# Kernel optimization log

Hardware: AMD Instinct MI355X
Metric: run time of the kernel (lower is better)

## Reference

```python
import jax, jax.numpy as jnp
import numpy as np

EMBED_DIM = 1024
NUM_HEADS = 16
HEAD_DIM = EMBED_DIM // NUM_HEADS
N_PATCHES = 220
ROPE_BASE = 10000.0
EPS = 1e-6


def rms_norm(x, g):
    # x: [..., d]
    rms = jnp.sqrt(jnp.mean(x * x, axis=-1, keepdims=True) + EPS)
    return g * (x / rms)


def apply_rope(x):
    # torchtune-style interleaved RoPE. x: [b, s, h, d]
    b, s, h, d = x.shape
    theta = 1.0 / (ROPE_BASE ** (jnp.arange(0, d, 2, dtype=jnp.float32) / d))  # [d/2]
    ang = jnp.arange(s, dtype=jnp.float32)[:, None] * theta[None, :]           # [s, d/2]
    cos = jnp.cos(ang)[None, :, None, :]
    sin = jnp.sin(ang)[None, :, None, :]
    xs = x.reshape(b, s, h, d // 2, 2)
    x0, x1 = xs[..., 0], xs[..., 1]
    out = jnp.stack([x0 * cos - x1 * sin, x1 * cos + x0 * sin], axis=-1)
    return out.reshape(b, s, h, d).astype(x.dtype)


def attention_block(x, w_qkv, w_proj, b_proj, q_gain, k_gain):
    # x: [N, S, C]; one SDPA branch (shared by spatial & temporal paths)
    N, S, C = x.shape
    H, D = NUM_HEADS, HEAD_DIM
    qkv = jnp.einsum('nsc,ec->nse', x, w_qkv).reshape(N, S, 3, H, D)
    q, k, v = qkv[:, :, 0], qkv[:, :, 1], qkv[:, :, 2]  # [N, S, H, D]
    q = apply_rope(rms_norm(q, q_gain))
    k = apply_rope(rms_norm(k, k_gain))
    scale = 1.0 / jnp.sqrt(jnp.float32(D))
    scores = jnp.einsum('nqhd,nkhd->nhqk', q, k) * scale
    attn = jax.nn.softmax(scores, axis=-1)
    out = jnp.einsum('nhqk,nkhd->nqhd', attn, v).reshape(N, S, C)
    return jnp.einsum('nsc,ec->nse', out, w_proj) + b_proj


def setup_inputs() -> dict:
    key = jax.random.key(0)
    ks = jax.random.split(key, 8)
    E = EMBED_DIM
    sd = 1.0 / np.sqrt(E)
    x = jax.random.normal(ks[0], (4, 5280, E), dtype=jnp.float32)
    w_sqkv = jax.random.uniform(ks[1], (3 * E, E), jnp.float32, -sd, sd)
    w_sproj = jax.random.uniform(ks[2], (E, E), jnp.float32, -sd, sd)
    b_sproj = jax.random.uniform(ks[3], (E,), jnp.float32, -sd, sd)
    w_tqkv = jax.random.uniform(ks[4], (3 * E, E), jnp.float32, -sd, sd)
    w_tproj = jax.random.uniform(ks[5], (E, E), jnp.float32, -sd, sd)
    b_tproj = jax.random.uniform(ks[6], (E,), jnp.float32, -sd, sd)
    g = jnp.ones((HEAD_DIM,), jnp.float32)
    return {
        'x': x,
        'w_sqkv': w_sqkv, 'w_sproj': w_sproj, 'b_sproj': b_sproj,
        'w_tqkv': w_tqkv, 'w_tproj': w_tproj, 'b_tproj': b_tproj,
        'sq_gain': g, 'sk_gain': g, 'tq_gain': g, 'tk_gain': g,
    }


def reference(x, w_sqkv, w_sproj, b_sproj, w_tqkv, w_tproj, b_tproj,
              sq_gain, sk_gain, tq_gain, tk_gain):
    B, T, C = x.shape
    P = N_PATCHES
    F = T // P
    # spatial attention per frame: (b f) p c
    xs = x.reshape(B, F, P, C).reshape(B * F, P, C)
    out_s = attention_block(xs, w_sqkv, w_sproj, b_sproj, sq_gain, sk_gain)
    # temporal attention per patch: (b p) f c
    xt = out_s.reshape(B, F, P, C).transpose(0, 2, 1, 3).reshape(B * P, F, C)
    out_t = attention_block(xt, w_tqkv, w_tproj, b_tproj, tq_gain, tk_gain)
    # (b p) f c -> b (f p) c
    out = out_t.reshape(B, P, F, C).transpose(0, 2, 1, 3).reshape(B, F * P, C)
    return out
```

## Files before the change

### kernel.cpp

```cpp
#include <hip/hip_runtime.h>

typedef _Float16 f16;
typedef _Float16 f16x8 __attribute__((ext_vector_type(8)));
typedef f16x8 f16x8a __attribute__((may_alias));
typedef float f32x4 __attribute__((ext_vector_type(4)));

#define NTOK 21120
#define MPAD 21248
#define SCALE_Q 0.18033688f

__device__ __forceinline__ void gll16(const void* g, void* l) {
  __builtin_amdgcn_global_load_lds(
      (const __attribute__((address_space(1))) unsigned int*)g,
      (__attribute__((address_space(3))) unsigned int*)l, 16, 0, 0);
}

__device__ __forceinline__ unsigned int pack2(float a, float b) {
  union { f16 h[2]; unsigned int u; } c;
  c.h[0] = (f16)a; c.h[1] = (f16)b;
  return c.u;
}
__device__ __forceinline__ unsigned short f2h(float a) {
  union { f16 h; unsigned short u; } c; c.h = (f16)a; return c.u;
}

template <int C>
__device__ __forceinline__ float dppf(float x) {
  union { float f; int i; } u, r;
  u.f = x;
  r.i = __builtin_amdgcn_update_dpp(0, u.i, C, 0xf, 0xf, true);
  return r.f;
}

__global__ __launch_bounds__(256) void cast_kernel(
    const float* __restrict__ in, unsigned short* __restrict__ out, int n4) {
  int i = blockIdx.x * 256 + threadIdx.x;
  if (i >= n4) return;
  float4 v = ((const float4*)in)[i];
  uint2 o;
  o.x = pack2(v.x, v.y);
  o.y = pack2(v.z, v.w);
  ((uint2*)out)[i] = o;
}

__global__ __launch_bounds__(256) void transpose_cast_kernel(
    const float* __restrict__ in, unsigned short* __restrict__ out) {
  __shared__ float tile[32][33];
  int bx = blockIdx.x & 31, by = blockIdx.x >> 5;
  int tx = threadIdx.x & 31, ty = threadIdx.x >> 5;
#pragma unroll
  for (int i = 0; i < 32; i += 8)
    tile[ty + i][tx] = in[(size_t)(by * 32 + ty + i) * 1024 + bx * 32 + tx];
  __syncthreads();
#pragma unroll
  for (int i = 0; i < 32; i += 8)
    out[(size_t)(bx * 32 + ty + i) * 1024 + by * 32 + tx] = f2h(tile[tx][ty + i]);
}

__global__ __launch_bounds__(256) void bias_combine_kernel(
    const float* __restrict__ w, const float* __restrict__ b, float* __restrict__ bc) {
  int e = blockIdx.x * 256 + threadIdx.x;
  if (e >= 3072) return;
  const float4* wr = (const float4*)(w + (size_t)e * 1024);
  const float4* b4 = (const float4*)b;
  float s = 0.f;
  for (int c = 0; c < 256; ++c) {
    float4 wv = wr[c], bv = b4[c];
    s += wv.x * bv.x + wv.y * bv.y + wv.z * bv.z + wv.w * bv.w;
  }
  bc[e] = s;
}

__global__ __launch_bounds__(256) void rope_table_kernel(float2* tabS, float2* tabT) {
  int t = blockIdx.x * 256 + threadIdx.x;
  const float lb = logf(10000.0f) * (1.0f / 32.0f);
  if (t < 220 * 32) {
    int s = t >> 5, i = t & 31;
    float theta = expf(-(float)i * lb);
    float ang = (float)s * theta;
    tabS[t] = make_float2(cosf(ang), sinf(ang));
  } else if (t < 220 * 32 + 24 * 32) {
    int u = t - 220 * 32;
    int s = u >> 5, i = u & 31;
    float theta = expf(-(float)i * lb);
    float ang = (float)s * theta;
    tabT[u] = make_float2(cosf(ang), sinf(ang));
  }
}

__global__ __launch_bounds__(256) void gemm_bt(
    const unsigned short* __restrict__ A, const unsigned short* __restrict__ B,
    const float* __restrict__ bias, void* __restrict__ C,
    int M, int N, int K, int outmode,
    const float2* __restrict__ tab, const float* __restrict__ gq,
    const float* __restrict__ gk, int mode) {
  __shared__ __align__(16) unsigned short sh[16384];
  unsigned short* As = sh;
  unsigned short* Bs = sh + 8192;
  const int tid = threadIdx.x;
  const int w = tid >> 6, lane = tid & 63;
  const int l15 = lane & 15, quad = lane >> 4;
  const int wr = w >> 1, wc = w & 1;

  const int ntn = N >> 7;
  const int stride = ntn << 3;
  const int g = blockIdx.x / stride, r = blockIdx.x % stride;
  const int tn = r % ntn, tm = g * 8 + r / ntn;

  f32x4 acc[4][4];
#pragma unroll
  for (int a = 0; a < 4; ++a)
#pragma unroll
    for (int b = 0; b < 4; ++b) acc[a][b] = (f32x4){0.f, 0.f, 0.f, 0.f};

  const int srow = tid >> 3;
  const int schk = tid & 7;
  const size_t arow0 = (size_t)tm * 128;
  const size_t brow0 = (size_t)tn * 128;
  const int nk = K >> 6;

  for (int kt = 0; kt < nk; ++kt) {
    __syncthreads();
    const int kb = kt << 6;
#pragma unroll
    for (int rd = 0; rd < 4; ++rd) {
      int row = rd * 32 + srow;
      int sc = (schk ^ (row & 7)) * 8;
      gll16(A + (arow0 + row) * K + kb + sc, (char*)As + rd * 4096 + tid * 16);
      gll16(B + (brow0 + row) * K + kb + sc, (char*)Bs + rd * 4096 + tid * 16);
    }
    __syncthreads();
#pragma unroll
    for (int kk = 0; kk < 2; ++kk) {
      f16x8 af[4], bf[4];
#pragma unroll
      for (int mt = 0; mt < 4; ++mt) {
        int ra = wr * 64 + mt * 16 + l15;
        af[mt] = *(const f16x8a*)((const char*)As + ra * 128 + (((kk * 4 + quad) ^ (ra & 7)) * 16));
        int rb = wc * 64 + mt * 16 + l15;
        bf[mt] = *(const f16x8a*)((const char*)Bs + rb * 128 + (((kk * 4 + quad) ^ (rb & 7)) * 16));
      }
#pragma unroll
      for (int mt = 0; mt < 4; ++mt)
#pragma unroll
        for (int nt = 0; nt < 4; ++nt)
          acc[mt][nt] = __builtin_amdgcn_mfma_f32_16x16x32_f16(af[mt], bf[nt], acc[mt][nt], 0, 0, 0);
    }
  }

  unsigned short* Cs = (unsigned short*)C;
#pragma unroll
  for (int p = 0; p < 2; ++p) {
    __syncthreads();
#pragma unroll
    for (int mi = 0; mi < 2; ++mi) {
      int mt = p * 2 + mi;
      int rl = wr * 32 + mi * 16 + quad * 4;
#pragma unroll
      for (int nt = 0; nt < 4; ++nt) {
        int cl = wc * 64 + nt * 16 + l15;
#pragma unroll
        for (int rg = 0; rg < 4; ++rg)
          sh[(rl + rg) * 136 + cl] = f2h(acc[mt][nt][rg]);
      }
    }
    __syncthreads();
#pragma unroll
    for (int c = 0; c < 4; ++c) {
      int rl = c * 16 + (tid >> 4), cx = tid & 15;
      int grow = tm * 128 + ((rl >> 5) << 6) + p * 32 + (rl & 31);
      uint4 v = *(const uint4*)&sh[rl * 136 + cx * 8];
      *(uint4*)&Cs[(size_t)grow * N + tn * 128 + cx * 8] = v;
    }
  }
}

#define FENCE() asm volatile("" ::: "memory")
#define BAR() do { FENCE(); __builtin_amdgcn_s_barrier(); FENCE(); } while (0)
#define WAITV(N) asm volatile("s_waitcnt vmcnt(" #N ")" ::: "memory")
#define WAITL(N) do { asm volatile("s_waitcnt lgkmcnt(" #N ")" ::: "memory"); \
                      __builtin_amdgcn_sched_barrier(0); } while (0)
#define ASLOT(T) (((T) % 3) * 32768)
#define BSLOT(T) (98304 + ((T) & 1) * 32768)
#define LDAf(T, mt, kk) (*(const f16x8a*)(smem + ASLOT(T) + wrOff + (mt) * 2048 + (aoff ^ ((kk) << 6))))
#define LDBf(T, nt, kk) (*(const f16x8a*)(smem + BSLOT(T) + bcOff + (nt) * 2048 + (aoff ^ ((kk) << 6))))
#define STAGE_A2(T, h) do { \
    gll16(aSp + (size_t)((h) * 128) * K + (T) * 64, smem + ASLOT(T) + (h) * 16384 + tid * 16); \
    gll16(aSp + (size_t)((h) * 128 + 64) * K + (T) * 64, smem + ASLOT(T) + (h) * 16384 + 8192 + tid * 16); \
  } while (0)
#define STAGE_B2(T, h) do { \
    gll16(bSp + (size_t)((h) * 128) * K + (T) * 64, smem + BSLOT(T) + (h) * 16384 + tid * 16); \
    gll16(bSp + (size_t)((h) * 128 + 64) * K + (T) * 64, smem + BSLOT(T) + (h) * 16384 + 8192 + tid * 16); \
  } while (0)
#define MM16(QB, A0_, A1_, A2_, A3_, B0_, B1_, B2_, B3_) do { \
    acc[QB + 0][0] = __builtin_amdgcn_mfma_f32_16x16x32_f16(A0_, B0_, acc[QB + 0][0], 0, 0, 0); \
    acc[QB + 0][1] = __builtin_amdgcn_mfma_f32_16x16x32_f16(A0_, B1_, acc[QB + 0][1], 0, 0, 0); \
    acc[QB + 0][2] = __builtin_amdgcn_mfma_f32_16x16x32_f16(A0_, B2_, acc[QB + 0][2], 0, 0, 0); \
    acc[QB + 0][3] = __builtin_amdgcn_mfma_f32_16x16x32_f16(A0_, B3_, acc[QB + 0][3], 0, 0, 0); \
    acc[QB + 1][0] = __builtin_amdgcn_mfma_f32_16x16x32_f16(A1_, B0_, acc[QB + 1][0], 0, 0, 0); \
    acc[QB + 1][1] = __builtin_amdgcn_mfma_f32_16x16x32_f16(A1_, B1_, acc[QB + 1][1], 0, 0, 0); \
    acc[QB + 1][2] = __builtin_amdgcn_mfma_f32_16x16x32_f16(A1_, B2_, acc[QB + 1][2], 0, 0, 0); \
    acc[QB + 1][3] = __builtin_amdgcn_mfma_f32_16x16x32_f16(A1_, B3_, acc[QB + 1][3], 0, 0, 0); \
    acc[QB + 2][0] = __builtin_amdgcn_mfma_f32_16x16x32_f16(A2_, B0_, acc[QB + 2][0], 0, 0, 0); \
    acc[QB + 2][1] = __builtin_amdgcn_mfma_f32_16x16x32_f16(A2_, B1_, acc[QB + 2][1], 0, 0, 0); \
    acc[QB + 2][2] = __builtin_amdgcn_mfma_f32_16x16x32_f16(A2_, B2_, acc[QB + 2][2], 0, 0, 0); \
    acc[QB + 2][3] = __builtin_amdgcn_mfma_f32_16x16x32_f16(A2_, B3_, acc[QB + 2][3], 0, 0, 0); \
    acc[QB + 3][0] = __builtin_amdgcn_mfma_f32_16x16x32_f16(A3_, B0_, acc[QB + 3][0], 0, 0, 0); \
    acc[QB + 3][1] = __builtin_amdgcn_mfma_f32_16x16x32_f16(A3_, B1_, acc[QB + 3][1], 0, 0, 0); \
    acc[QB + 3][2] = __builtin_amdgcn_mfma_f32_16x16x32_f16(A3_, B2_, acc[QB + 3][2], 0, 0, 0); \
    acc[QB + 3][3] = __builtin_amdgcn_mfma_f32_16x16x32_f16(A3_, B3_, acc[QB + 3][3], 0, 0, 0); \
  } while (0)

__global__ __launch_bounds__(512, 2) void gemm256(
    const unsigned short* __restrict__ A, const unsigned short* __restrict__ B,
    const float* __restrict__ bias, void* __restrict__ C,
    int M, int N, int K, int outmode,
    const float2* __restrict__ tab, const float* __restrict__ gq,
    const float* __restrict__ gk, int mode) {
  extern __shared__ char smem[];
  const int tid = threadIdx.x;
  const int w = tid >> 6, lane = tid & 63;
  const int l15 = lane & 15, quad = lane >> 4;
  const int wr = w >> 2, wc = w & 3;

  const int nwg = gridDim.x;
  const int qd = nwg >> 3, rm = nwg & 7;
  const int xcd = blockIdx.x & 7, lin = blockIdx.x >> 3;
  const int wgid = (xcd < rm ? xcd * (qd + 1) : rm * (qd + 1) + (xcd - rm) * qd) + lin;
  const int ntn = N >> 8;
  const int stg = ntn << 3;
  const int g = wgid / stg, r2 = wgid % stg;
  const int tn = r2 % ntn, tm = g * 8 + r2 / ntn;

  const int wrOff = wr * 16384;
  const int bcOff = (wc >> 1) * 16384 + (wc & 1) * 8192;
  const int aoff = l15 * 128 + ((quad ^ (l15 & 7)) << 4);

  const int sc = ((tid & 7) ^ ((tid >> 3) & 7)) * 8;
  const unsigned short* aSp = A + (size_t)(tm * 256 + (tid >> 3)) * K + sc;
  const unsigned short* bSp = B + (size_t)(tn * 256 + (tid >> 3)) * K + sc;

  f32x4 acc[8][4];
#pragma unroll
  for (int i = 0; i < 8; ++i)
#pragma unroll
    for (int j = 0; j < 4; ++j) acc[i][j] = (f32x4){0.f, 0.f, 0.f, 0.f};

  STAGE_A2(0, 0); STAGE_A2(0, 1);
  STAGE_B2(0, 0); STAGE_B2(0, 1);
  STAGE_A2(1, 0); STAGE_A2(1, 1);
  WAITV(4);
  BAR();

#pragma unroll
  for (int t = 0; t < 16; ++t) {
    f16x8 bA0, bA1, bA2, bA3, bB0, bB1, bB2, bB3;
    f16x8 aA0, aA1, aA2, aA3, aB0, aB1, aB2, aB3;
    f16x8 aC0, aC1, aC2, aC3, aD0, aD1, aD2, aD3;
    bA0 = LDBf(t, 0, 0); bA1 = LDBf(t, 1, 0); bA2 = LDBf(t, 2, 0); bA3 = LDBf(t, 3, 0);
    aA0 = LDAf(t, 0, 0); aA1 = LDAf(t, 1, 0); aA2 = LDAf(t, 2, 0); aA3 = LDAf(t, 3, 0);
    aB0 = LDAf(t, 4, 0); aB1 = LDAf(t, 5, 0); aB2 = LDAf(t, 6, 0); aB3 = LDAf(t, 7, 0);
    if (t <= 14) { STAGE_B2(t + 1, 0); STAGE_B2(t + 1, 1); }
    WAITL(4);
    __builtin_amdgcn_s_setprio(1);
    MM16(0, aA0, aA1, aA2, aA3, bA0, bA1, bA2, bA3);
    __builtin_amdgcn_s_setprio(0);
    bB0 = LDBf(t, 0, 1); bB1 = LDBf(t, 1, 1); bB2 = LDBf(t, 2, 1); bB3 = LDBf(t, 3, 1);
    aC0 = LDAf(t, 0, 1); aC1 = LDAf(t, 1, 1); aC2 = LDAf(t, 2, 1); aC3 = LDAf(t, 3, 1);
    WAITL(8);
    __builtin_amdgcn_s_setprio(1);
    MM16(4, aB0, aB1, aB2, aB3, bA0, bA1, bA2, bA3);
    __builtin_amdgcn_s_setprio(0);
    aD0 = LDAf(t, 4, 1); aD1 = LDAf(t, 5, 1); aD2 = LDAf(t, 6, 1); aD3 = LDAf(t, 7, 1);
    if (t <= 13) { STAGE_A2(t + 2, 0); STAGE_A2(t + 2, 1); }
    WAITL(4);
    __builtin_amdgcn_s_setprio(1);
    MM16(0, aC0, aC1, aC2, aC3, bB0, bB1, bB2, bB3);
    __builtin_amdgcn_s_setprio(0);
    WAITL(0);
    __builtin_amdgcn_s_setprio(1);
    MM16(4, aD0, aD1, aD2, aD3, bB0, bB1, bB2, bB3);
    __builtin_amdgcn_s_setprio(0);
    if (t <= 13) { WAITV(4); } else if (t == 14) { WAITV(0); }
    BAR();
  }

  const size_t grow0 = (size_t)tm * 256 + wr * 128;
  const int gcol0 = tn * 256 + wc * 64;

  float bl[4] = {0.f, 0.f, 0.f, 0.f};
  if (bias != nullptr) {
#pragma unroll
    for (int nt = 0; nt < 4; ++nt) bl[nt] = bias[gcol0 + nt * 16 + l15];
  }

  if (outmode == 2) {
    float* wf = (float*)(smem + w * 16384);
    const int frow = lane >> 4, fc = lane & 15;
#pragma unroll
    for (int h = 0; h < 2; ++h) {
#pragma unroll
      for (int mi = 0; mi < 4; ++mi)
#pragma unroll
        for (int nt = 0; nt < 4; ++nt)
#pragma unroll
          for (int rg = 0; rg < 4; ++rg) {
            int row = mi * 16 + quad * 4 + rg;
            int col = nt * 16 + l15;
            int c = col >> 2, lo = col & 3;
            wf[row * 64 + ((c ^ (row & 15)) << 2) + lo] = acc[h * 4 + mi][nt][rg] + bl[nt];
          }
#pragma unroll
      for (int it = 0; it < 16; ++it) {
        int row = it * 4 + frow;
        float4 v = *(const float4*)(wf + row * 64 + ((fc ^ (row & 15)) << 2));
        size_t gr = grow0 + h * 64 + row;
        if (gr < (size_t)M)
          *(float4*)((float*)C + gr * N + gcol0 + fc * 4) = v;
      }
    }
    return;
  }

  unsigned short* wh = (unsigned short*)(smem + w * 16384);
  if (outmode == 3 && tn < 8) {
    const int isQ = tn < 4;
    const float* gg = isQ ? gq : gk;
    float gv[4];
#pragma unroll
    for (int nt = 0; nt < 4; ++nt) gv[nt] = gg[nt * 16 + l15];
#pragma unroll
    for (int mt = 0; mt < 8; ++mt) {
      float v[4][4], rr[4];
#pragma unroll
      for (int rg = 0; rg < 4; ++rg) rr[rg] = 0.f;
#pragma unroll
      for (int nt = 0; nt < 4; ++nt)
#pragma unroll
        for (int rg = 0; rg < 4; ++rg) {
          float x = acc[mt][nt][rg] + bl[nt];
          v[nt][rg] = x;
          rr[rg] += x * x;
        }
#pragma unroll
      for (int rg = 0; rg < 4; ++rg) {
        float s = rr[rg];
        s += dppf<0xB1>(s);
        s += dppf<0x4E>(s);
        s += dppf<0x141>(s);
        s += dppf<0x140>(s);
        float r = rsqrtf(s * (1.0f / 64.0f) + 1e-6f);
        rr[rg] = isQ ? r * SCALE_Q : r;
      }
      int pos[4];
#pragma unroll
      for (int rg = 0; rg < 4; ++rg) {
        int grow = (int)grow0 + mt * 16 + quad * 4 + rg;
        pos[rg] = mode ? ((grow / 220) % 24) : (grow % 220);
      }
#pragma unroll
      for (int nt = 0; nt < 4; ++nt) {
        int col = nt * 16 + l15;
        int ii = nt * 8 + (l15 >> 1);
        int c = col >> 3, lo = col & 7;
#pragma unroll
        for (int rg = 0; rg < 4; ++rg) {
          float2 cs = tab[pos[rg] * 32 + ii];
          float x = v[nt][rg] * rr[rg] * gv[nt];
          float p = dppf<0xB1>(x);
          float o = (l15 & 1) ? (x * cs.x + p * cs.y) : (x * cs.x - p * cs.y);
          int row = mt * 16 + quad * 4 + rg;
          wh[row * 64 + ((c ^ (row & 7)) << 3) + lo] = f2h(o);
        }
      }
    }
  } else {
#pragma unroll
    for (int mt = 0; mt < 8; ++mt)
#pragma unroll
      for (int nt = 0; nt < 4; ++nt) {
        int col = nt * 16 + l15;
        int c = col >> 3, lo = col & 7;
#pragma unroll
        for (int rg = 0; rg < 4; ++rg) {
          int row = mt * 16 + quad * 4 + rg;
          wh[row * 64 + ((c ^ (row & 7)) << 3) + lo] = f2h(acc[mt][nt][rg] + bl[nt]);
        }
      }
  }
  {
    const int frow = lane >> 3, fch = lane & 7;
    unsigned short* C16 = (unsigned short*)C;
#pragma unroll
    for (int it = 0; it < 16; ++it) {
      int row = it * 8 + frow;
      uint4 vv = *(const uint4*)((const char*)wh + row * 128 + ((fch ^ (row & 7)) << 4));
      size_t gr = grow0 + row;
      if (gr < (size_t)M)
        *(uint4*)(C16 + gr * N + gcol0 + fch * 8) = vv;
    }
  }
}

__global__ __launch_bounds__(256) void attn_spatial(
    const unsigned short* __restrict__ qkv, unsigned short* __restrict__ aout) {
  __shared__ __align__(16) unsigned short sh[30720];
  unsigned short* Kls = sh;
  unsigned short* Vt = sh + 8192;
  unsigned short* P = sh + 22528;
  const int tid = threadIdx.x;
  const int w = tid >> 6, lane = tid & 63;
  const int l15 = lane & 15, quad = lane >> 4;
  const int n = blockIdx.x >> 4, h = blockIdx.x & 15;
  const size_t tb = (size_t)n * 220;
  const unsigned short* qbase = qkv + tb * 3072 + h * 64;

  f16x8 aq[4][2];
#pragma unroll
  for (int mt = 0; mt < 4; ++mt) {
    int row = w * 64 + mt * 16 + l15;
    if (row > 219) row = 219;
#pragma unroll
    for (int c = 0; c < 2; ++c)
      aq[mt][c] = *(const f16x8a*)(qbase + (size_t)row * 3072 + c * 32 + quad * 8);
  }
  if (tid < 220) {
    const uint4* src = (const uint4*)(qbase + (size_t)tid * 3072 + 2048);
    uint4 vv[8];
#pragma unroll
    for (int c = 0; c < 8; ++c) vv[c] = src[c];
    const unsigned short* us = (const unsigned short*)vv;
#pragma unroll
    for (int d = 0; d < 64; ++d) Vt[d * 224 + tid] = us[d];
  } else if (tid < 224) {
#pragma unroll
    for (int d = 0; d < 64; ++d) Vt[d * 224 + tid] = 0;
  }

  float lsum[4][4];
  f32x4 o[4][4];
#pragma unroll
  for (int mt = 0; mt < 4; ++mt)
#pragma unroll
    for (int rg = 0; rg < 4; ++rg) lsum[mt][rg] = 0.f;
#pragma unroll
  for (int mt = 0; mt < 4; ++mt)
#pragma unroll
    for (int nt = 0; nt < 4; ++nt) o[mt][nt] = (f32x4){0.f, 0.f, 0.f, 0.f};

  const int xr = (l15 & 3) ^ ((l15 >> 2) & 3);
  unsigned short* Pw = P + w * 2048;

  for (int half = 0; half < 2; ++half) {
    const int k0 = half * 128;
    const int nslot = half ? 736 : 1024;
#pragma unroll
    for (int k = 0; k < 4; ++k) {
      int slot = k * 256 + tid;
      if (slot < nslot) {
        int rl = slot >> 3, c = slot & 7;
        gll16(qbase + (size_t)(k0 + rl) * 3072 + 1024 + ((c ^ (rl & 7)) * 8),
              (char*)Kls + k * 4096 + w * 1024);
      }
    }
    __syncthreads();
    const int nci = half ? 3 : 4;
    for (int ci = 0; ci < nci; ++ci) {
      const int cig = half * 4 + ci;
      f16x8 bk[2][2];
#pragma unroll
      for (int ct = 0; ct < 2; ++ct) {
        int rl = ci * 32 + ct * 16 + l15;
#pragma unroll
        for (int c = 0; c < 2; ++c)
          bk[ct][c] = *(const f16x8a*)((const char*)Kls + rl * 128 + (((quad + 4 * c) ^ (rl & 7)) * 16));
      }
      f32x4 sc[4][2];
#pragma unroll
      for (int mt = 0; mt < 4; ++mt)
#pragma unroll
        for (int ct = 0; ct < 2; ++ct) {
          f32x4 z = (f32x4){0.f, 0.f, 0.f, 0.f};
          z = __builtin_amdgcn_mfma_f32_16x16x32_f16(aq[mt][0], bk[ct][0], z, 0, 0, 0);
          sc[mt][ct] = __builtin_amdgcn_mfma_f32_16x16x32_f16(aq[mt][1], bk[ct][1], z, 0, 0, 0);
        }
      const int okk = (cig * 32 + 16 + l15) < 220;
#pragma unroll
      for (int mt = 0; mt < 4; ++mt)
#pragma unroll
        for (int rg = 0; rg < 4; ++rg) {
          float p0 = exp2f(sc[mt][0][rg]);
          float p1 = okk ? exp2f(sc[mt][1][rg]) : 0.0f;
          lsum[mt][rg] += p0 + p1;
          int xw = quad ^ rg;
          unsigned short* pb = Pw + (mt * 16 + quad * 4 + rg) * 32;
          pb[(((l15 >> 3) ^ xw) * 8) + (l15 & 7)] = f2h(p0);
          pb[(((2 + (l15 >> 3)) ^ xw) * 8) + (l15 & 7)] = f2h(p1);
        }
      __asm__ volatile("s_waitcnt lgkmcnt(0)" ::: "memory");
      f16x8 ap[4], bv[4];
#pragma unroll
      for (int mt = 0; mt < 4; ++mt)
        ap[mt] = *(const f16x8a*)((const char*)Pw + (mt * 16 + l15) * 64 + (quad ^ xr) * 16);
#pragma unroll
      for (int nt = 0; nt < 4; ++nt)
        bv[nt] = *(const f16x8a*)((const char*)Vt + (nt * 16 + l15) * 448 + cig * 64 + quad * 16);
#pragma unroll
      for (int mt = 0; mt < 4; ++mt)
#pragma unroll
        for (int nt = 0; nt < 4; ++nt)
          o[mt][nt] = __builtin_amdgcn_mfma_f32_16x16x32_f16(ap[mt], bv[nt], o[mt][nt], 0, 0, 0);
    }
    __syncthreads();
  }

#pragma unroll
  for (int mt = 0; mt < 4; ++mt)
#pragma unroll
    for (int rg = 0; rg < 4; ++rg) {
      float l = lsum[mt][rg];
      l += __shfl_xor(l, 1);
      l += __shfl_xor(l, 2);
      l += __shfl_xor(l, 4);
      l += __shfl_xor(l, 8);
      int s = w * 64 + mt * 16 + quad * 4 + rg;
      if (s < 220) {
        float inv = 1.0f / l;
        unsigned short* dst = aout + (tb + s) * 1024 + h * 64;
#pragma unroll
        for (int nt = 0; nt < 4; ++nt) dst[nt * 16 + l15] = f2h(o[mt][nt][rg] * inv);
      }
    }
}

__global__ __launch_bounds__(256) void attn_temporal(
    const unsigned short* __restrict__ qkv, unsigned short* __restrict__ aout) {
  __shared__ __align__(16) unsigned short sh[14336];
  const int tid = threadIdx.x;
  const int w = tid >> 6, lane = tid & 63;
  const int l15 = lane & 15, quad = lane >> 4;
  const int b = blockIdx.x / 880;
  const int rem = blockIdx.x % 880;
  const int p = rem >> 2, hq = rem & 3;
  const int h = hq * 4 + w;
  unsigned short* Vtw = sh + w * 2560;
  unsigned short* Pw = sh + 10240 + w * 1024;
  const unsigned short* base = qkv + ((size_t)(b * 24) * 220 + p) * 3072 + h * 64;
  const size_t fs = (size_t)220 * 3072;

  {
    int r = lane >> 1, hf = lane & 1;
    if (r < 24) {
      const uint4* src = (const uint4*)(base + r * fs + 2048 + hf * 32);
      uint4 vv[4];
#pragma unroll
      for (int c = 0; c < 4; ++c) vv[c] = src[c];
      const unsigned short* us = (const unsigned short*)vv;
#pragma unroll
      for (int j = 0; j < 32; ++j) Vtw[(hf * 32 + j) * 40 + r] = us[j];
    } else {
#pragma unroll
      for (int j = 0; j < 32; ++j) Vtw[(hf * 32 + j) * 40 + r] = 0;
    }
  }
  f16x8 aq[2][2], bk[2][2];
#pragma unroll
  for (int mt = 0; mt < 2; ++mt) {
    int row = mt * 16 + l15;
    if (row > 23) row = 23;
#pragma unroll
    for (int c = 0; c < 2; ++c)
      aq[mt][c] = *(const f16x8a*)(base + row * fs + c * 32 + quad * 8);
  }
#pragma unroll
  for (int ct = 0; ct < 2; ++ct) {
    int row = ct * 16 + l15;
    if (row > 23) row = 23;
#pragma unroll
    for (int c = 0; c < 2; ++c)
      bk[ct][c] = *(const f16x8a*)(base + row * fs + 1024 + c * 32 + quad * 8);
  }
  f32x4 sc[2][2];
#pragma unroll
  for (int mt = 0; mt < 2; ++mt)
#pragma unroll
    for (int ct = 0; ct < 2; ++ct) {
      f32x4 z = (f32x4){0.f, 0.f, 0.f, 0.f};
      z = __builtin_amdgcn_mfma_f32_16x16x32_f16(aq[mt][0], bk[ct][0], z, 0, 0, 0);
      sc[mt][ct] = __builtin_amdgcn_mfma_f32_16x16x32_f16(aq[mt][1], bk[ct][1], z, 0, 0, 0);
    }
  const int xr = (l15 & 3) ^ ((l15 >> 2) & 3);
  const int okk = l15 < 8;
  float lr[2][4];
#pragma unroll
  for (int mt = 0; mt < 2; ++mt)
#pragma unroll
    for (int rg = 0; rg < 4; ++rg) {
      float p0 = exp2f(sc[mt][0][rg]);
      float p1 = okk ? exp2f(sc[mt][1][rg]) : 0.0f;
      float rs = p0 + p1;
      rs += __shfl_xor(rs, 1);
      rs += __shfl_xor(rs, 2);
      rs += __shfl_xor(rs, 4);
      rs += __shfl_xor(rs, 8);
      lr[mt][rg] = rs;
      int xw = quad ^ rg;
      unsigned short* pb = Pw + (mt * 16 + quad * 4 + rg) * 32;
      pb[(((l15 >> 3) ^ xw) * 8) + (l15 & 7)] = f2h(p0);
      pb[(((2 + (l15 >> 3)) ^ xw) * 8) + (l15 & 7)] = f2h(p1);
    }
  __asm__ volatile("s_waitcnt lgkmcnt(0)" ::: "memory");
  f16x8 ap[2], bv[4];
#pragma unroll
  for (int mt = 0; mt < 2; ++mt)
    ap[mt] = *(const f16x8a*)((const char*)Pw + (mt * 16 + l15) * 64 + (quad ^ xr) * 16);
#pragma unroll
  for (int nt = 0; nt < 4; ++nt)
    bv[nt] = *(const f16x8a*)((const char*)Vtw + (nt * 16 + l15) * 80 + quad * 16);
  f32x4 o[2][4];
#pragma unroll
  for (int mt = 0; mt < 2; ++mt)
#pragma unroll
    for (int nt = 0; nt < 4; ++nt) {
      f32x4 z = (f32x4){0.f, 0.f, 0.f, 0.f};
      o[mt][nt] = __builtin_amdgcn_mfma_f32_16x16x32_f16(ap[mt], bv[nt], z, 0, 0, 0);
    }
#pragma unroll
  for (int mt = 0; mt < 2; ++mt)
#pragma unroll
    for (int rg = 0; rg < 4; ++rg) {
      int s = mt * 16 + quad * 4 + rg;
      if (s < 24) {
        float inv = 1.0f / lr[mt][rg];
        unsigned short* dst = aout + ((size_t)(b * 24 + s) * 220 + p) * 1024 + h * 64;
#pragma unroll
        for (int nt = 0; nt < 4; ++nt) dst[nt * 16 + l15] = f2h(o[mt][nt][rg] * inv);
      }
    }
}

extern "C" void kernel_launch(void* const* d_in, const int* in_sizes, int n_in,
                              void* d_out, int out_size, void* d_ws, size_t ws_size,
                              hipStream_t stream) {
  (void)in_sizes; (void)n_in; (void)out_size; (void)ws_size;
  const float* x = (const float*)d_in[0];
  const float* wsqkv = (const float*)d_in[1];
  const float* wsproj = (const float*)d_in[2];
  const float* bsproj = (const float*)d_in[3];
  const float* wtqkv = (const float*)d_in[4];
  const float* wtproj = (const float*)d_in[5];
  const float* btproj = (const float*)d_in[6];
  const float* sqg = (const float*)d_in[7];
  const float* skg = (const float*)d_in[8];
  const float* tqg = (const float*)d_in[9];
  const float* tkg = (const float*)d_in[10];

  static bool attr_done = false;
  if (!attr_done) {
    hipFuncSetAttribute(reinterpret_cast<const void*>(gemm256),
                        hipFuncAttributeMaxDynamicSharedMemorySize, 163840);
    attr_done = true;
  }

  char* ws = (char*)d_ws;
  size_t off = 0;
  auto alloc = [&](size_t bytes) {
    char* ptr = ws + off;
    off += (bytes + 255) & ~(size_t)255;
    return ptr;
  };
  unsigned short* xb = (unsigned short*)alloc((size_t)MPAD * 1024 * 2);
  unsigned short* qkvb = (unsigned short*)alloc((size_t)NTOK * 3072 * 2);
  unsigned short* aoutb = (unsigned short*)alloc((size_t)MPAD * 1024 * 2);
  unsigned short* wsqkvb = (unsigned short*)alloc((size_t)3072 * 1024 * 2);
  unsigned short* wsprojTb = (unsigned short*)alloc((size_t)1024 * 1024 * 2);
  unsigned short* wtqkvb = (unsigned short*)alloc((size_t)3072 * 1024 * 2);
  unsigned short* wtprojb = (unsigned short*)alloc((size_t)1024 * 1024 * 2);
  unsigned short* wcb = (unsigned short*)alloc((size_t)3072 * 1024 * 2);
  float* bcb = (float*)alloc(3072 * 4);
  float2* tabS = (float2*)alloc(220 * 32 * 8);
  float2* tabT = (float2*)alloc(24 * 32 * 8);

  hipMemsetAsync(xb + (size_t)NTOK * 1024, 0, (size_t)(MPAD - NTOK) * 1024 * 2, stream);
  hipMemsetAsync(aoutb + (size_t)NTOK * 1024, 0, (size_t)(MPAD - NTOK) * 1024 * 2, stream);

  dim3 blk(256);
  cast_kernel<<<21120, blk, 0, stream>>>(x, xb, 5406720);
  cast_kernel<<<3072, blk, 0, stream>>>(wsqkv, wsqkvb, 786432);
  cast_kernel<<<3072, blk, 0, stream>>>(wtqkv, wtqkvb, 786432);
  cast_kernel<<<1024, blk, 0, stream>>>(wtproj, wtprojb, 262144);
  transpose_cast_kernel<<<1024, blk, 0, stream>>>(wsproj, wsprojTb);
  bias_combine_kernel<<<12, blk, 0, stream>>>(wtqkv, bsproj, bcb);
  rope_table_kernel<<<31, blk, 0, stream>>>(tabS, tabT);

  gemm_bt<<<dim3(24 * 8), blk, 0, stream>>>(wtqkvb, wsprojTb, nullptr, wcb, 3072, 1024, 1024, 0,
                                            nullptr, nullptr, nullptr, 0);

  dim3 blk512(512);
  gemm256<<<dim3(83 * 12), blk512, 163840, stream>>>(xb, wsqkvb, nullptr, qkvb, NTOK, 3072, 1024, 3,
                                                     tabS, sqg, skg, 0);
  attn_spatial<<<dim3(1536), blk, 0, stream>>>(qkvb, aoutb);
  gemm256<<<dim3(83 * 12), blk512, 163840, stream>>>(aoutb, wcb, bcb, qkvb, NTOK, 3072, 1024, 3,
                                                     tabT, tqg, tkg, 1);
  attn_temporal<<<dim3(3520), blk, 0, stream>>>(qkvb, aoutb);
  gemm256<<<dim3(83 * 4), blk512, 163840, stream>>>(aoutb, wtprojb, btproj, (float*)d_out,
                                                    NTOK, 1024, 1024, 2,
                                                    nullptr, nullptr, nullptr, 0);
}
```

Measured before the change: 722.5 us.

## Make QKV GEMMs persistent over four column tiles, prefetching next tile during epilogue

The two QKV GEMMs now launch 249 workgroups, each computing four consecutive 256-wide column tiles for one row tile, instead of 996 single-tile workgroups. The first K-stages of the next tile are issued before the current tile's epilogue so loads overlap the RMSNorm/RoPE and store work. The epilogue is restructured to use a smaller per-wave LDS scratch region at a fixed offset so it does not clobber the prefetched buffers. The aim is to cut workgroup launch and prologue cost and hide epilogue latency. The cost is fewer workgroups (about one per CU), so load balance and latency hiding within the CU may suffer.

```diff
diff --git a/kernel.cpp b/kernel.cpp
--- a/kernel.cpp
+++ b/kernel.cpp
@@ -188,9 +188,9 @@
     gll16(aSp + (size_t)((h) * 128) * K + (T) * 64, smem + ASLOT(T) + (h) * 16384 + tid * 16); \
     gll16(aSp + (size_t)((h) * 128 + 64) * K + (T) * 64, smem + ASLOT(T) + (h) * 16384 + 8192 + tid * 16); \
   } while (0)
-#define STAGE_B2(T, h) do { \
-    gll16(bSp + (size_t)((h) * 128) * K + (T) * 64, smem + BSLOT(T) + (h) * 16384 + tid * 16); \
-    gll16(bSp + (size_t)((h) * 128 + 64) * K + (T) * 64, smem + BSLOT(T) + (h) * 16384 + 8192 + tid * 16); \
+#define STAGE_B2(P, T, h) do { \
+    gll16((P) + (size_t)((h) * 128) * K + (T) * 64, smem + BSLOT(T) + (h) * 16384 + tid * 16); \
+    gll16((P) + (size_t)((h) * 128 + 64) * K + (T) * 64, smem + BSLOT(T) + (h) * 16384 + 8192 + tid * 16); \
   } while (0)
 #define MM16(QB, A0_, A1_, A2_, A3_, B0_, B1_, B2_, B3_) do { \
     acc[QB + 0][0] = __builtin_amdgcn_mfma_f32_16x16x32_f16(A0_, B0_, acc[QB + 0][0], 0, 0, 0); \
@@ -216,7 +216,7 @@
     const float* __restrict__ bias, void* __restrict__ C,
     int M, int N, int K, int outmode,
     const float2* __restrict__ tab, const float* __restrict__ gq,
-    const float* __restrict__ gk, int mode) {
+    const float* __restrict__ gk, int mode, int cpb) {
   extern __shared__ char smem[];
   const int tid = threadIdx.x;
   const int w = tid >> 6, lane = tid & 63;
@@ -227,10 +227,16 @@
   const int qd = nwg >> 3, rm = nwg & 7;
   const int xcd = blockIdx.x & 7, lin = blockIdx.x >> 3;
   const int wgid = (xcd < rm ? xcd * (qd + 1) : rm * (qd + 1) + (xcd - rm) * qd) + lin;
-  const int ntn = N >> 8;
-  const int stg = ntn << 3;
-  const int g = wgid / stg, r2 = wgid % stg;
-  const int tn = r2 % ntn, tm = g * 8 + r2 / ntn;
+  int tm, tn0;
+  if (cpb > 1) {
+    tm = wgid % 83;
+    tn0 = (wgid / 83) * cpb;
+  } else {
+    const int ntn = N >> 8;
+    const int stg = ntn << 3;
+    const int g = wgid / stg, r2 = wgid % stg;
+    tn0 = r2 % ntn; tm = g * 8 + r2 / ntn;
+  }
 
   const int wrOff = wr * 16384;
   const int bcOff = (wc >> 1) * 16384 + (wc & 1) * 8192;
@@ -238,166 +244,194 @@
 
   const int sc = ((tid & 7) ^ ((tid >> 3) & 7)) * 8;
   const unsigned short* aSp = A + (size_t)(tm * 256 + (tid >> 3)) * K + sc;
-  const unsigned short* bSp = B + (size_t)(tn * 256 + (tid >> 3)) * K + sc;
-
-  f32x4 acc[8][4];
-#pragma unroll
-  for (int i = 0; i < 8; ++i)
-#pragma unroll
-    for (int j = 0; j < 4; ++j) acc[i][j] = (f32x4){0.f, 0.f, 0.f, 0.f};
+  const unsigned short* bSp = B + (size_t)(tn0 * 256 + (tid >> 3)) * K + sc;
+
+  const size_t grow0 = (size_t)tm * 256 + wr * 128;
+  unsigned short* C16 = (unsigned short*)C;
 
   STAGE_A2(0, 0); STAGE_A2(0, 1);
-  STAGE_B2(0, 0); STAGE_B2(0, 1);
+  STAGE_B2(bSp, 0, 0); STAGE_B2(bSp, 0, 1);
   STAGE_A2(1, 0); STAGE_A2(1, 1);
   WAITV(4);
   BAR();
 
-#pragma unroll
-  for (int t = 0; t < 16; ++t) {
-    f16x8 bA0, bA1, bA2, bA3, bB0, bB1, bB2, bB3;
-    f16x8 aA0, aA1, aA2, aA3, aB0, aB1, aB2, aB3;
-    f16x8 aC0, aC1, aC2, aC3, aD0, aD1, aD2, aD3;
-    bA0 = LDBf(t, 0, 0); bA1 = LDBf(t, 1, 0); bA2 = LDBf(t, 2, 0); bA3 = LDBf(t, 3, 0);
-    aA0 = LDAf(t, 0, 0); aA1 = LDAf(t, 1, 0); aA2 = LDAf(t, 2, 0); aA3 = LDAf(t, 3, 0);
-    aB0 = LDAf(t, 4, 0); aB1 = LDAf(t, 5, 0); aB2 = LDAf(t, 6, 0); aB3 = LDAf(t, 7, 0);
-    if (t <= 14) { STAGE_B2(t + 1, 0); STAGE_B2(t + 1, 1); }
-    WAITL(4);
-    __builtin_amdgcn_s_setprio(1);
-    MM16(0, aA0, aA1, aA2, aA3, bA0, bA1, bA2, bA3);
-    __builtin_amdgcn_s_setprio(0);
-    bB0 = LDBf(t, 0, 1); bB1 = LDBf(t, 1, 1); bB2 = LDBf(t, 2, 1); bB3 = LDBf(t, 3, 1);
-    aC0 = LDAf(t, 0, 1); aC1 = LDAf(t, 1, 1); aC2 = LDAf(t, 2, 1); aC3 = LDAf(t, 3, 1);
-    WAITL(8);
-    __builtin_amdgcn_s_setprio(1);
-    MM16(4, aB0, aB1, aB2, aB3, bA0, bA1, bA2, bA3);
-    __builtin_amdgcn_s_setprio(0);
-    aD0 = LDAf(t, 4, 1); aD1 = LDAf(t, 5, 1); aD2 = LDAf(t, 6, 1); aD3 = LDAf(t, 7, 1);
-    if (t <= 13) { STAGE_A2(t + 2, 0); STAGE_A2(t + 2, 1); }
-    WAITL(4);
-    __builtin_amdgcn_s_setprio(1);
-    MM16(0, aC0, aC1, aC2, aC3, bB0, bB1, bB2, bB3);
-    __builtin_amdgcn_s_setprio(0);
-    WAITL(0);
-    __builtin_amdgcn_s_setprio(1);
-    MM16(4, aD0, aD1, aD2, aD3, bB0, bB1, bB2, bB3);
-    __builtin_amdgcn_s_setprio(0);
-    if (t <= 13) { WAITV(4); } else if (t == 14) { WAITV(0); }
-    BAR();
-  }
-
-  const size_t grow0 = (size_t)tm * 256 + wr * 128;
-  const int gcol0 = tn * 256 + wc * 64;
-
-  float bl[4] = {0.f, 0.f, 0.f, 0.f};
-  if (bias != nullptr) {
-#pragma unroll
-    for (int nt = 0; nt < 4; ++nt) bl[nt] = bias[gcol0 + nt * 16 + l15];
-  }
-
-  if (outmode == 2) {
-    float* wf = (float*)(smem + w * 16384);
-    const int frow = lane >> 4, fc = lane & 15;
-#pragma unroll
-    for (int h = 0; h < 2; ++h) {
-#pragma unroll
-      for (int mi = 0; mi < 4; ++mi)
+  for (int c = 0; c < cpb; ++c) {
+    const int tn = tn0 + c;
+    f32x4 acc[8][4];
+#pragma unroll
+    for (int i = 0; i < 8; ++i)
+#pragma unroll
+      for (int j = 0; j < 4; ++j) acc[i][j] = (f32x4){0.f, 0.f, 0.f, 0.f};
+
+#pragma unroll
+    for (int t = 0; t < 16; ++t) {
+      f16x8 bA0, bA1, bA2, bA3, bB0, bB1, bB2, bB3;
+      f16x8 aA0, aA1, aA2, aA3, aB0, aB1, aB2, aB3;
+      f16x8 aC0, aC1, aC2, aC3, aD0, aD1, aD2, aD3;
+      bA0 = LDBf(t, 0, 0); bA1 = LDBf(t, 1, 0); bA2 = LDBf(t, 2, 0); bA3 = LDBf(t, 3, 0);
+      aA0 = LDAf(t, 0, 0); aA1 = LDAf(t, 1, 0); aA2 = LDAf(t, 2, 0); aA3 = LDAf(t, 3, 0);
+      aB0 = LDAf(t, 4, 0); aB1 = LDAf(t, 5, 0); aB2 = LDAf(t, 6, 0); aB3 = LDAf(t, 7, 0);
+      if (t <= 14) { STAGE_B2(bSp, t + 1, 0); STAGE_B2(bSp, t + 1, 1); }
+      WAITL(4);
+      __builtin_amdgcn_s_setprio(1);
+      MM16(0, aA0, aA1, aA2, aA3, bA0, bA1, bA2, bA3);
+      __builtin_amdgcn_s_setprio(0);
+      bB0 = LDBf(t, 0, 1); bB1 = LDBf(t, 1, 1); bB2 = LDBf(t, 2, 1); bB3 = LDBf(t, 3, 1);
+      aC0 = LDAf(t, 0, 1); aC1 = LDAf(t, 1, 1); aC2 = LDAf(t, 2, 1); aC3 = LDAf(t, 3, 1);
+      WAITL(8);
+      __builtin_amdgcn_s_setprio(1);
+      MM16(4, aB0, aB1, aB2, aB3, bA0, bA1, bA2, bA3);
+      __builtin_amdgcn_s_setprio(0);
+      aD0 = LDAf(t, 4, 1); aD1 = LDAf(t, 5, 1); aD2 = LDAf(t, 6, 1); aD3 = LDAf(t, 7, 1);
+      if (t <= 13) { STAGE_A2(t + 2, 0); STAGE_A2(t + 2, 1); }
+      WAITL(4);
+      __builtin_amdgcn_s_setprio(1);
+      MM16(0, aC0, aC1, aC2, aC3, bB0, bB1, bB2, bB3);
+      __builtin_amdgcn_s_setprio(0);
+      WAITL(0);
+      __builtin_amdgcn_s_setprio(1);
+      MM16(4, aD0, aD1, aD2, aD3, bB0, bB1, bB2, bB3);
+      __builtin_amdgcn_s_setprio(0);
+      if (t <= 13) { WAITV(4); } else if (t == 14) { WAITV(0); }
+      BAR();
+    }
+
+    const unsigned short* bSpN = bSp + (size_t)256 * K;
+    if (c + 1 < cpb) {
+      STAGE_A2(0, 0); STAGE_A2(0, 1);
+      STAGE_B2(bSpN, 0, 0); STAGE_B2(bSpN, 0, 1);
+      STAGE_A2(1, 0); STAGE_A2(1, 1);
+    }
+
+    const int gcol0 = tn * 256 + wc * 64;
+    float bl[4] = {0.f, 0.f, 0.f, 0.f};
+    if (bias != nullptr) {
+#pragma unroll
+      for (int nt = 0; nt < 4; ++nt) bl[nt] = bias[gcol0 + nt * 16 + l15];
+    }
+
+    if (outmode == 2) {
+      float* wf = (float*)(smem + 65536 + w * 4096);
+      const int frw = lane >> 4, fc = lane & 15;
+#pragma unroll
+      for (int mt = 0; mt < 8; ++mt) {
 #pragma unroll
         for (int nt = 0; nt < 4; ++nt)
 #pragma unroll
           for (int rg = 0; rg < 4; ++rg) {
-            int row = mi * 16 + quad * 4 + rg;
+            int rl = quad * 4 + rg;
             int col = nt * 16 + l15;
-            int c = col >> 2, lo = col & 3;
-            wf[row * 64 + ((c ^ (row & 15)) << 2) + lo] = acc[h * 4 + mi][nt][rg] + bl[nt];
+            int cq = col >> 2, lo = col & 3;
+            wf[rl * 64 + ((cq ^ rl) << 2) + lo] = acc[mt][nt][rg] + bl[nt];
           }
 #pragma unroll
-      for (int it = 0; it < 16; ++it) {
-        int row = it * 4 + frow;
-        float4 v = *(const float4*)(wf + row * 64 + ((fc ^ (row & 15)) << 2));
-        size_t gr = grow0 + h * 64 + row;
-        if (gr < (size_t)M)
-          *(float4*)((float*)C + gr * N + gcol0 + fc * 4) = v;
-      }
-    }
-    return;
-  }
-
-  unsigned short* wh = (unsigned short*)(smem + w * 16384);
-  if (outmode == 3 && tn < 8) {
-    const int isQ = tn < 4;
-    const float* gg = isQ ? gq : gk;
-    float gv[4];
-#pragma unroll
-    for (int nt = 0; nt < 4; ++nt) gv[nt] = gg[nt * 16 + l15];
-#pragma unroll
-    for (int mt = 0; mt < 8; ++mt) {
-      float v[4][4], rr[4];
-#pragma unroll
-      for (int rg = 0; rg < 4; ++rg) rr[rg] = 0.f;
-#pragma unroll
-      for (int nt = 0; nt < 4; ++nt)
-#pragma unroll
-        for (int rg = 0; rg < 4; ++rg) {
-          float x = acc[mt][nt][rg] + bl[nt];
-          v[nt][rg] = x;
-          rr[rg] += x * x;
-        }
-#pragma unroll
-      for (int rg = 0; rg < 4; ++rg) {
-        float s = rr[rg];
-        s += dppf<0xB1>(s);
-        s += dppf<0x4E>(s);
-        s += dppf<0x141>(s);
-        s += dppf<0x140>(s);
-        float r = rsqrtf(s * (1.0f / 64.0f) + 1e-6f);
-        rr[rg] = isQ ? r * SCALE_Q : r;
-      }
-      int pos[4];
-#pragma unroll
-      for (int rg = 0; rg < 4; ++rg) {
-        int grow = (int)grow0 + mt * 16 + quad * 4 + rg;
-        pos[rg] = mode ? ((grow / 220) % 24) : (grow % 220);
-      }
-#pragma unroll
-      for (int nt = 0; nt < 4; ++nt) {
-        int col = nt * 16 + l15;
-        int ii = nt * 8 + (l15 >> 1);
-        int c = col >> 3, lo = col & 7;
-#pragma unroll
-        for (int rg = 0; rg < 4; ++rg) {
-          float2 cs = tab[pos[rg] * 32 + ii];
-          float x = v[nt][rg] * rr[rg] * gv[nt];
-          float p = dppf<0xB1>(x);
-          float o = (l15 & 1) ? (x * cs.x + p * cs.y) : (x * cs.x - p * cs.y);
-          int row = mt * 16 + quad * 4 + rg;
-          wh[row * 64 + ((c ^ (row & 7)) << 3) + lo] = f2h(o);
+        for (int it = 0; it < 4; ++it) {
+          int rl = it * 4 + frw;
+          float4 v = *(const float4*)(wf + rl * 64 + ((fc ^ rl) << 2));
+          size_t gr = grow0 + mt * 16 + rl;
+          if (gr < (size_t)M)
+            *(float4*)((float*)C + gr * N + gcol0 + fc * 4) = v;
         }
       }
-    }
-  } else {
-#pragma unroll
-    for (int mt = 0; mt < 8; ++mt)
-#pragma unroll
-      for (int nt = 0; nt < 4; ++nt) {
-        int col = nt * 16 + l15;
-        int c = col >> 3, lo = col & 7;
-#pragma unroll
-        for (int rg = 0; rg < 4; ++rg) {
-          int row = mt * 16 + quad * 4 + rg;
-          wh[row * 64 + ((c ^ (row & 7)) << 3) + lo] = f2h(acc[mt][nt][rg] + bl[nt]);
+    } else {
+      unsigned short* wh = (unsigned short*)(smem + 65536 + w * 4096);
+      const int frow = lane >> 3, fch = lane & 7;
+      if (outmode == 3 && tn < 8) {
+        const int isQ = tn < 4;
+        const float* gg = isQ ? gq : gk;
+        float gv[4];
+#pragma unroll
+        for (int nt = 0; nt < 4; ++nt) gv[nt] = gg[nt * 16 + l15];
+#pragma unroll
+        for (int mp = 0; mp < 4; ++mp) {
+#pragma unroll
+          for (int mi = 0; mi < 2; ++mi) {
+            const int mt = mp * 2 + mi;
+            float v[4][4], rr[4];
+#pragma unroll
+            for (int rg = 0; rg < 4; ++rg) rr[rg] = 0.f;
+#pragma unroll
+            for (int nt = 0; nt < 4; ++nt)
+#pragma unroll
+              for (int rg = 0; rg < 4; ++rg) {
+                float x = acc[mt][nt][rg] + bl[nt];
+                v[nt][rg] = x;
+                rr[rg] += x * x;
+              }
+#pragma unroll
+            for (int rg = 0; rg < 4; ++rg) {
+              float s = rr[rg];
+              s += dppf<0xB1>(s);
+              s += dppf<0x4E>(s);
+              s += dppf<0x141>(s);
+              s += dppf<0x140>(s);
+              float r = rsqrtf(s * (1.0f / 64.0f) + 1e-6f);
+              rr[rg] = isQ ? r * SCALE_Q : r;
+            }
+            int pos[4];
+#pragma unroll
+            for (int rg = 0; rg < 4; ++rg) {
+              int grow = (int)grow0 + mt * 16 + quad * 4 + rg;
+              pos[rg] = mode ? ((grow / 220) % 24) : (grow % 220);
+            }
+#pragma unroll
+            for (int nt = 0; nt < 4; ++nt) {
+              int col = nt * 16 + l15;
+              int ii = nt * 8 + (l15 >> 1);
+              int cc = col >> 3, lo = col & 7;
+#pragma unroll
+              for (int rg = 0; rg < 4; ++rg) {
+                float2 cs = tab[pos[rg] * 32 + ii];
+                float x = v[nt][rg] * rr[rg] * gv[nt];
+                float p = dppf<0xB1>(x);
+                float o = (l15 & 1) ? (x * cs.x + p * cs.y) : (x * cs.x - p * cs.y);
+                int rl = mi * 16 + quad * 4 + rg;
+                wh[rl * 64 + ((cc ^ (rl & 7)) << 3) + lo] = f2h(o);
+              }
+            }
+          }
+#pragma unroll
+          for (int it = 0; it < 4; ++it) {
+            int rl = it * 8 + frow;
+            uint4 vv = *(const uint4*)((const char*)wh + rl * 128 + ((fch ^ (rl & 7)) << 4));
+            size_t gr = grow0 + mp * 32 + rl;
+            if (gr < (size_t)M)
+              *(uint4*)(C16 + gr * N + gcol0 + fch * 8) = vv;
+          }
+        }
+      } else {
+#pragma unroll
+        for (int mp = 0; mp < 4; ++mp) {
+#pragma unroll
+          for (int mi = 0; mi < 2; ++mi) {
+            const int mt = mp * 2 + mi;
+#pragma unroll
+            for (int nt = 0; nt < 4; ++nt) {
+              int col = nt * 16 + l15;
+              int cc = col >> 3, lo = col & 7;
+#pragma unroll
+              for (int rg = 0; rg < 4; ++rg) {
+                int rl = mi * 16 + quad * 4 + rg;
+                wh[rl * 64 + ((cc ^ (rl & 7)) << 3) + lo] = f2h(acc[mt][nt][rg] + bl[nt]);
+              }
+            }
+          }
+#pragma unroll
+          for (int it = 0; it < 4; ++it) {
+            int rl = it * 8 + frow;
+            uint4 vv = *(const uint4*)((const char*)wh + rl * 128 + ((fch ^ (rl & 7)) << 4));
+            size_t gr = grow0 + mp * 32 + rl;
+            if (gr < (size_t)M)
+              *(uint4*)(C16 + gr * N + gcol0 + fch * 8) = vv;
+          }
         }
       }
-  }
-  {
-    const int frow = lane >> 3, fch = lane & 7;
-    unsigned short* C16 = (unsigned short*)C;
-#pragma unroll
-    for (int it = 0; it < 16; ++it) {
-      int row = it * 8 + frow;
-      uint4 vv = *(const uint4*)((const char*)wh + row * 128 + ((fch ^ (row & 7)) << 4));
-      size_t gr = grow0 + row;
-      if (gr < (size_t)M)
-        *(uint4*)(C16 + gr * N + gcol0 + fch * 8) = vv;
+    }
+
+    if (c + 1 < cpb) {
+      bSp = bSpN;
+      WAITV(4);
+      BAR();
     }
   }
 }
@@ -697,13 +731,13 @@
                                             nullptr, nullptr, nullptr, 0);
 
   dim3 blk512(512);
-  gemm256<<<dim3(83 * 12), blk512, 163840, stream>>>(xb, wsqkvb, nullptr, qkvb, NTOK, 3072, 1024, 3,
-                                                     tabS, sqg, skg, 0);
+  gemm256<<<dim3(249), blk512, 163840, stream>>>(xb, wsqkvb, nullptr, qkvb, NTOK, 3072, 1024, 3,
+                                                 tabS, sqg, skg, 0, 4);
   attn_spatial<<<dim3(1536), blk, 0, stream>>>(qkvb, aoutb);
-  gemm256<<<dim3(83 * 12), blk512, 163840, stream>>>(aoutb, wcb, bcb, qkvb, NTOK, 3072, 1024, 3,
-                                                     tabT, tqg, tkg, 1);
+  gemm256<<<dim3(249), blk512, 163840, stream>>>(aoutb, wcb, bcb, qkvb, NTOK, 3072, 1024, 3,
+                                                 tabT, tqg, tkg, 1, 4);
   attn_temporal<<<dim3(3520), blk, 0, stream>>>(qkvb, aoutb);
   gemm256<<<dim3(83 * 4), blk512, 163840, stream>>>(aoutb, wtprojb, btproj, (float*)d_out,
                                                     NTOK, 1024, 1024, 2,
-                                                    nullptr, nullptr, nullptr, 0);
-}
+                                                    nullptr, nullptr, nullptr, 0, 1);
+}
```

Measured after the change: 1.457 ms. +101.6%, slower.
